# Kernel optimization log

Hardware: AMD Instinct MI355X
Metric: run time of the kernel (lower is better)

The kernel has to match this reference:

```python
import jax, jax.numpy as jnp
import numpy as np

BATCH = 16384
NUM_Q = 100000
NUM_TAGS = 1024
DIFF_FEAT = 3
DIM = 64
HIDDEN = 128


def setup_inputs() -> dict:
    key = jax.random.key(0)
    ks = jax.random.split(key, 10)
    questions = jax.random.randint(ks[0], (BATCH,), 0, NUM_Q, dtype=jnp.int64 if jax.config.jax_enable_x64 else jnp.int32)
    question_skill_targets = jax.random.randint(ks[1], (BATCH, NUM_TAGS), 0, 2, dtype=jnp.int32)
    difficulty_feats = jax.random.normal(ks[2], (BATCH, DIFF_FEAT), dtype=jnp.float32)
    Q_emb = jax.random.normal(ks[3], (NUM_Q, DIM), dtype=jnp.float32) * 0.02
    S_emb = jax.random.normal(ks[4], (NUM_TAGS, DIM), dtype=jnp.float32) * 0.02
    W_diff = jax.random.normal(ks[5], (DIFF_FEAT, DIM), dtype=jnp.float32) * 0.1
    b_diff = jnp.zeros((DIM,), dtype=jnp.float32)
    W_fc = jax.random.normal(ks[6], (3 * DIM + 3, HIDDEN), dtype=jnp.float32) * 0.05
    b_fc = jnp.zeros((HIDDEN,), dtype=jnp.float32)
    W_out = jax.random.normal(ks[7], (HIDDEN, 1), dtype=jnp.float32) * 0.05
    b_out = jnp.zeros((1,), dtype=jnp.float32)
    return {"questions": questions, "question_skill_targets": question_skill_targets,
            "difficulty_feats": difficulty_feats, "Q_emb": Q_emb, "S_emb": S_emb,
            "W_diff": W_diff, "b_diff": b_diff, "W_fc": W_fc, "b_fc": b_fc,
            "W_out": W_out, "b_out": b_out}


def reference(questions, question_skill_targets, difficulty_feats,
              Q_emb, S_emb, W_diff, b_diff, W_fc, b_fc, W_out, b_out):
    # Ragged segment-mean over skill sets: mean of skill embeddings whose
    # multi-hot entry is nonzero == (T @ S) / count per row.
    t = question_skill_targets.astype(jnp.float32)            # [B, T]
    counts = jnp.sum(t, axis=1, keepdims=True)                # [B, 1] (>=1 w.h.p.)
    mu_skill = (t @ S_emb) / counts                           # [B, D]
    q = Q_emb[questions]                                      # [B, D]
    a = difficulty_feats @ W_diff + b_diff                    # [B, D]
    # PNN product layer: pairwise inner products + concat linear signals
    p12 = jnp.sum(q * mu_skill, axis=-1, keepdims=True)
    p13 = jnp.sum(q * a, axis=-1, keepdims=True)
    p23 = jnp.sum(mu_skill * a, axis=-1, keepdims=True)
    z = jnp.concatenate([q, mu_skill, a, p12, p13, p23], axis=-1)  # [B, 3D+3]
    e = jax.nn.relu(z @ W_fc + b_fc)                          # [B, H]
    p = jax.nn.sigmoid(e @ W_out + b_out)[:, 0]               # [B]
    return (e, p)
```

## Files before the change

kernel.cpp:

```cpp
#include <hip/hip_runtime.h>
#include <hip/hip_bf16.h>

#define BATCH   16384
#define NTAGS   1024
#define DIM     64
#define HID     128

typedef __attribute__((ext_vector_type(8)))  short bf16x8;
typedef __attribute__((ext_vector_type(4)))  float f32x4;
typedef __attribute__((ext_vector_type(16))) float f32x16;

__device__ __forceinline__ unsigned short f2bf(float v) {
    unsigned u = __builtin_bit_cast(unsigned, v);
    return (unsigned short)((u + 0x7FFFu + ((u >> 16) & 1u)) >> 16);
}
__device__ __forceinline__ float bf2f(unsigned short u) {
    return __builtin_bit_cast(float, ((unsigned)u) << 16);
}

__global__ __launch_bounds__(256) void prep_pack32(const float* __restrict__ S,
                                                   const float* __restrict__ Wfc,
                                                   unsigned short* __restrict__ Sp32,
                                                   unsigned short* __restrict__ Wp)
{
    int tid = blockIdx.x * 256 + threadIdx.x;
    if (tid < 65536) {
        int k = tid >> 6, d = tid & 63;
        float v = S[tid];
        int ks = k >> 4, j = k & 7, kh = (k >> 3) & 1;
        int nf = d >> 5, lane = (d & 31) + 32 * kh;
        Sp32[((size_t)(ks * 2 + nf) * 64 + lane) * 8 + j] = f2bf(v);
    } else if (tid < 65536 + 24576) {
        int t2 = tid - 65536;
        int k = t2 >> 7, col = t2 & 127;
        float v = Wfc[t2];
        int kt = k >> 5, j = k & 7, l = ((k >> 3) & 3) * 16 + (col & 15), ct = col >> 4;
        Wp[((size_t)(kt * 8 + ct) * 64 + l) * 8 + j] = f2bf(v);
    }
}

__global__ __launch_bounds__(256) void gemm32(const int* __restrict__ T,
                                              const unsigned short* __restrict__ Sp32,
                                              unsigned short* __restrict__ musum_p,
                                              float* __restrict__ cntp)
{
    const int lane = threadIdx.x & 63;
    const int wid  = threadIdx.x >> 6;
    const int gw   = blockIdx.x * 4 + wid;
    const int mt   = gw >> 2;
    const int ksp  = gw & 3;
    const int r32  = lane & 31;
    const int kh   = lane >> 5;

    const int* tp = T + (size_t)(mt * 32 + r32) * 1024 + ksp * 256 + kh * 8;
    const unsigned short* spb = Sp32 + (size_t)(ksp * 16) * 1024 + lane * 8;

    f32x16 acc0{}, acc1{};
    int c = 0;
#pragma unroll
    for (int st = 0; st < 16; ++st) {
        int4 t0 = *(const int4*)(tp + st * 16);
        int4 t1 = *(const int4*)(tp + st * 16 + 4);
        c += t0.x + t0.y + t0.z + t0.w + t1.x + t1.y + t1.z + t1.w;
        bf16x8 af;
        af[0] = (short)((-t0.x) & 0x3F80);
        af[1] = (short)((-t0.y) & 0x3F80);
        af[2] = (short)((-t0.z) & 0x3F80);
        af[3] = (short)((-t0.w) & 0x3F80);
        af[4] = (short)((-t1.x) & 0x3F80);
        af[5] = (short)((-t1.y) & 0x3F80);
        af[6] = (short)((-t1.z) & 0x3F80);
        af[7] = (short)((-t1.w) & 0x3F80);

        const unsigned short* s2 = spb + st * 1024;
        bf16x8 b0 = *(const bf16x8*)(s2);
        bf16x8 b1 = *(const bf16x8*)(s2 + 512);

        acc0 = __builtin_amdgcn_mfma_f32_32x32x16_bf16(af, b0, acc0, 0, 0, 0);
        acc1 = __builtin_amdgcn_mfma_f32_32x32x16_bf16(af, b1, acc1, 0, 0, 0);
    }

    c += __shfl_xor(c, 32);
    if (lane < 32) cntp[(size_t)(mt * 32 + lane) * 4 + ksp] = (float)c;

    unsigned short* mo = musum_p + (size_t)ksp * BATCH * 64;
#pragma unroll
    for (int reg = 0; reg < 16; ++reg) {
        int rr = (reg & 3) + 8 * (reg >> 2) + 4 * kh;
        size_t base = (size_t)(mt * 32 + rr) * 64 + r32;
        mo[base]      = f2bf(acc0[reg]);
        mo[base + 32] = f2bf(acc1[reg]);
    }
}

__global__ __launch_bounds__(256) void tail_kernel(
    const int* __restrict__ questions, const float* __restrict__ dfeat,
    const float* __restrict__ Qemb,
    const float* __restrict__ Wdiff, const float* __restrict__ bdiff,
    const float* __restrict__ Wfc, const float* __restrict__ bfc,
    const float* __restrict__ Wout, const float* __restrict__ bout,
    const unsigned short* __restrict__ musum_p, const float* __restrict__ cntp,
    const unsigned short* __restrict__ Wp,
    float* __restrict__ out_e, float* __restrict__ out_p)
{
    __shared__ alignas(16) unsigned short zb[16][200];
    __shared__ float scal[16][3];
    __shared__ float pacc[16][4];

    const int tid  = threadIdx.x;
    const int lane = tid & 63;
    const int wid  = tid >> 6;
    const int g    = lane >> 4;
    const int rl   = lane & 15;
    const int rb   = blockIdx.x * 16;

    {
        int r = tid >> 4, c16 = tid & 15, d0 = c16 * 4;
        int row = rb + r;

        float4 cp = *(const float4*)&cntp[(size_t)row * 4];
        float inv = 1.f / (cp.x + cp.y + cp.z + cp.w);

        float m0 = 0.f, m1 = 0.f, m2 = 0.f, m3 = 0.f;
#pragma unroll
        for (int p = 0; p < 4; ++p) {
            ushort4 mv = *(const ushort4*)&musum_p[((size_t)p * BATCH + row) * 64 + d0];
            m0 += bf2f(mv.x); m1 += bf2f(mv.y); m2 += bf2f(mv.z); m3 += bf2f(mv.w);
        }
        float mu[4] = {m0 * inv, m1 * inv, m2 * inv, m3 * inv};

        int qi = questions[row];
        float4 q4 = *(const float4*)(Qemb + (size_t)qi * 64 + d0);
        float q[4] = {q4.x, q4.y, q4.z, q4.w};

        float f0 = dfeat[row * 3 + 0];
        float f1 = dfeat[row * 3 + 1];
        float f2 = dfeat[row * 3 + 2];
        float aa[4];
#pragma unroll
        for (int d = 0; d < 4; ++d)
            aa[d] = bdiff[d0 + d] + f0 * Wdiff[d0 + d] + f1 * Wdiff[64 + d0 + d]
                  + f2 * Wdiff[128 + d0 + d];

        ushort4 qv, mv, av;
        qv.x = f2bf(q[0]);  qv.y = f2bf(q[1]);  qv.z = f2bf(q[2]);  qv.w = f2bf(q[3]);
        mv.x = f2bf(mu[0]); mv.y = f2bf(mu[1]); mv.z = f2bf(mu[2]); mv.w = f2bf(mu[3]);
        av.x = f2bf(aa[0]); av.y = f2bf(aa[1]); av.z = f2bf(aa[2]); av.w = f2bf(aa[3]);
        *(ushort4*)&zb[r][d0]       = qv;
        *(ushort4*)&zb[r][64 + d0]  = mv;
        *(ushort4*)&zb[r][128 + d0] = av;

        float s12 = 0.f, s13 = 0.f, s23 = 0.f;
#pragma unroll
        for (int d = 0; d < 4; ++d) {
            s12 += q[d] * mu[d];
            s13 += q[d] * aa[d];
            s23 += mu[d] * aa[d];
        }
#pragma unroll
        for (int off = 1; off < 16; off <<= 1) {
            s12 += __shfl_xor(s12, off);
            s13 += __shfl_xor(s13, off);
            s23 += __shfl_xor(s23, off);
        }
        if (c16 == 0) { scal[r][0] = s12; scal[r][1] = s13; scal[r][2] = s23; }
    }
    __syncthreads();

    {
        bf16x8 afr[6];
#pragma unroll
        for (int kt = 0; kt < 6; ++kt)
            afr[kt] = *(const bf16x8*)&zb[rl][kt * 32 + g * 8];

        float pr0 = 0.f, pr1 = 0.f, pr2 = 0.f, pr3 = 0.f;
#pragma unroll
        for (int c2 = 0; c2 < 2; ++c2) {
            int ct = wid * 2 + c2;
            f32x4 e{};
            const unsigned short* wp = Wp + (size_t)ct * 512 + lane * 8;
#pragma unroll
            for (int kt = 0; kt < 6; ++kt) {
                bf16x8 bfr = *(const bf16x8*)(wp + (size_t)kt * 4096);
                e = __builtin_amdgcn_mfma_f32_16x16x32_bf16(afr[kt], bfr, e, 0, 0, 0);
            }
            int h = ct * 16 + rl;
            float w192 = Wfc[192 * 128 + h];
            float w193 = Wfc[193 * 128 + h];
            float w194 = Wfc[194 * 128 + h];
            float bb = bfc[h];
            float wo = Wout[h];
#pragma unroll
            for (int r = 0; r < 4; ++r) {
                int row = g * 4 + r;
                float ev = e[r] + bb + scal[row][0] * w192 + scal[row][1] * w193
                         + scal[row][2] * w194;
                ev = ev > 0.f ? ev : 0.f;
                out_e[(size_t)(rb + row) * 128 + h] = ev;
                float pc = ev * wo;
                if (r == 0) pr0 += pc; else if (r == 1) pr1 += pc;
                else if (r == 2) pr2 += pc; else pr3 += pc;
            }
        }
#pragma unroll
        for (int off = 1; off < 16; off <<= 1) {
            pr0 += __shfl_xor(pr0, off);
            pr1 += __shfl_xor(pr1, off);
            pr2 += __shfl_xor(pr2, off);
            pr3 += __shfl_xor(pr3, off);
        }
        if (rl == 0) {
            pacc[g * 4 + 0][wid] = pr0;
            pacc[g * 4 + 1][wid] = pr1;
            pacc[g * 4 + 2][wid] = pr2;
            pacc[g * 4 + 3][wid] = pr3;
        }
    }
    __syncthreads();
    if (tid < 16) {
        float v = pacc[tid][0] + pacc[tid][1] + pacc[tid][2] + pacc[tid][3] + bout[0];
        out_p[rb + tid] = 1.f / (1.f + expf(-v));
    }
}

extern "C" void kernel_launch(void* const* d_in, const int* in_sizes, int n_in,
                              void* d_out, int out_size, void* d_ws, size_t ws_size,
                              hipStream_t stream)
{
    const int*   questions = (const int*)d_in[0];
    const int*   T         = (const int*)d_in[1];
    const float* dfeat     = (const float*)d_in[2];
    const float* Qemb      = (const float*)d_in[3];
    const float* Semb      = (const float*)d_in[4];
    const float* Wdiff     = (const float*)d_in[5];
    const float* bdiff     = (const float*)d_in[6];
    const float* Wfc       = (const float*)d_in[7];
    const float* bfc       = (const float*)d_in[8];
    const float* Wout      = (const float*)d_in[9];
    const float* bout      = (const float*)d_in[10];

    char* ws = (char*)d_ws;
    unsigned short* Sp32    = (unsigned short*)ws;
    unsigned short* Wp      = (unsigned short*)(ws + 131072);
    unsigned short* musum_p = (unsigned short*)(ws + 262144);
    float*          cntp    = (float*)(ws + 262144 + 8388608);

    float* out_e = (float*)d_out;
    float* out_p = out_e + (size_t)BATCH * HID;

    hipLaunchKernelGGL(prep_pack32, dim3(352), dim3(256), 0, stream, Semb, Wfc, Sp32, Wp);
    hipLaunchKernelGGL(gemm32, dim3(512), dim3(256), 0, stream, T, Sp32, musum_p, cntp);
    hipLaunchKernelGGL(tail_kernel, dim3(BATCH / 16), dim3(256), 0, stream,
                       questions, dfeat, Qemb, Wdiff, bdiff, Wfc, bfc, Wout, bout,
                       musum_p, cntp, Wp, out_e, out_p);
}
```

Measured before the change: 31.67 us.

## Fuse skill GEMM and MLP tail into one kernel with LDS partial sums

Merges the multi-hot-times-skill-embedding GEMM and the MLP tail into a single 512-thread kernel handling 32 rows per block. Eight waves each cover a 128-wide K slice and reduce their partial sums through LDS, so the bf16 partial-sum buffer no longer goes to global memory and one launch is removed. Question-embedding and difficulty-feature loads are issued before the GEMM to overlap their latency. In exchange there are fewer blocks (512), larger LDS use per block, and a barrier between the GEMM and tail phases.

```diff
diff --git a/kernel.cpp b/kernel.cpp
--- a/kernel.cpp
+++ b/kernel.cpp
@@ -39,108 +39,98 @@
     }
 }
 
-__global__ __launch_bounds__(256) void gemm32(const int* __restrict__ T,
-                                              const unsigned short* __restrict__ Sp32,
-                                              unsigned short* __restrict__ musum_p,
-                                              float* __restrict__ cntp)
-{
-    const int lane = threadIdx.x & 63;
-    const int wid  = threadIdx.x >> 6;
-    const int gw   = blockIdx.x * 4 + wid;
-    const int mt   = gw >> 2;
-    const int ksp  = gw & 3;
-    const int r32  = lane & 31;
-    const int kh   = lane >> 5;
-
-    const int* tp = T + (size_t)(mt * 32 + r32) * 1024 + ksp * 256 + kh * 8;
-    const unsigned short* spb = Sp32 + (size_t)(ksp * 16) * 1024 + lane * 8;
-
-    f32x16 acc0{}, acc1{};
-    int c = 0;
-#pragma unroll
-    for (int st = 0; st < 16; ++st) {
-        int4 t0 = *(const int4*)(tp + st * 16);
-        int4 t1 = *(const int4*)(tp + st * 16 + 4);
-        c += t0.x + t0.y + t0.z + t0.w + t1.x + t1.y + t1.z + t1.w;
-        bf16x8 af;
-        af[0] = (short)((-t0.x) & 0x3F80);
-        af[1] = (short)((-t0.y) & 0x3F80);
-        af[2] = (short)((-t0.z) & 0x3F80);
-        af[3] = (short)((-t0.w) & 0x3F80);
-        af[4] = (short)((-t1.x) & 0x3F80);
-        af[5] = (short)((-t1.y) & 0x3F80);
-        af[6] = (short)((-t1.z) & 0x3F80);
-        af[7] = (short)((-t1.w) & 0x3F80);
-
-        const unsigned short* s2 = spb + st * 1024;
-        bf16x8 b0 = *(const bf16x8*)(s2);
-        bf16x8 b1 = *(const bf16x8*)(s2 + 512);
-
-        acc0 = __builtin_amdgcn_mfma_f32_32x32x16_bf16(af, b0, acc0, 0, 0, 0);
-        acc1 = __builtin_amdgcn_mfma_f32_32x32x16_bf16(af, b1, acc1, 0, 0, 0);
-    }
-
-    c += __shfl_xor(c, 32);
-    if (lane < 32) cntp[(size_t)(mt * 32 + lane) * 4 + ksp] = (float)c;
-
-    unsigned short* mo = musum_p + (size_t)ksp * BATCH * 64;
-#pragma unroll
-    for (int reg = 0; reg < 16; ++reg) {
-        int rr = (reg & 3) + 8 * (reg >> 2) + 4 * kh;
-        size_t base = (size_t)(mt * 32 + rr) * 64 + r32;
-        mo[base]      = f2bf(acc0[reg]);
-        mo[base + 32] = f2bf(acc1[reg]);
-    }
-}
-
-__global__ __launch_bounds__(256) void tail_kernel(
-    const int* __restrict__ questions, const float* __restrict__ dfeat,
-    const float* __restrict__ Qemb,
+__global__ __launch_bounds__(512, 4) void fused_kernel(
+    const int* __restrict__ questions, const int* __restrict__ T,
+    const float* __restrict__ dfeat, const float* __restrict__ Qemb,
     const float* __restrict__ Wdiff, const float* __restrict__ bdiff,
     const float* __restrict__ Wfc, const float* __restrict__ bfc,
     const float* __restrict__ Wout, const float* __restrict__ bout,
-    const unsigned short* __restrict__ musum_p, const float* __restrict__ cntp,
-    const unsigned short* __restrict__ Wp,
+    const unsigned short* __restrict__ Sp32, const unsigned short* __restrict__ Wp,
     float* __restrict__ out_e, float* __restrict__ out_p)
 {
-    __shared__ alignas(16) unsigned short zb[16][200];
-    __shared__ float scal[16][3];
-    __shared__ float pacc[16][4];
+    __shared__ alignas(16) unsigned short accp[8][32][72];
+    __shared__ float cntp[8][32];
+    __shared__ alignas(16) unsigned short zb[32][200];
+    __shared__ float scal[32][3];
+    __shared__ float pacc[32][4];
 
     const int tid  = threadIdx.x;
     const int lane = tid & 63;
     const int wid  = tid >> 6;
+    const int r32  = lane & 31;
+    const int kh   = lane >> 5;
     const int g    = lane >> 4;
     const int rl   = lane & 15;
-    const int rb   = blockIdx.x * 16;
+    const int rb   = blockIdx.x * 32;
+
+    const int pr_r = tid >> 4, pr_c = tid & 15, pr_d0 = pr_c * 4;
+    const int qi = questions[rb + pr_r];
+    const float4 q4 = *(const float4*)(Qemb + (size_t)qi * 64 + pr_d0);
+    const float pf0 = dfeat[(rb + pr_r) * 3 + 0];
+    const float pf1 = dfeat[(rb + pr_r) * 3 + 1];
+    const float pf2 = dfeat[(rb + pr_r) * 3 + 2];
 
     {
-        int r = tid >> 4, c16 = tid & 15, d0 = c16 * 4;
-        int row = rb + r;
-
-        float4 cp = *(const float4*)&cntp[(size_t)row * 4];
-        float inv = 1.f / (cp.x + cp.y + cp.z + cp.w);
+        f32x16 acc0{}, acc1{};
+        int c = 0;
+        const int* tp = T + (size_t)(rb + r32) * 1024 + wid * 128 + kh * 8;
+        const unsigned short* spb = Sp32 + (size_t)(wid * 8) * 1024 + lane * 8;
+
+#pragma unroll
+        for (int st = 0; st < 8; ++st) {
+            int4 t0 = *(const int4*)(tp + st * 16);
+            int4 t1 = *(const int4*)(tp + st * 16 + 4);
+            c += t0.x + t0.y + t0.z + t0.w + t1.x + t1.y + t1.z + t1.w;
+            bf16x8 af;
+            af[0] = (short)((-t0.x) & 0x3F80);
+            af[1] = (short)((-t0.y) & 0x3F80);
+            af[2] = (short)((-t0.z) & 0x3F80);
+            af[3] = (short)((-t0.w) & 0x3F80);
+            af[4] = (short)((-t1.x) & 0x3F80);
+            af[5] = (short)((-t1.y) & 0x3F80);
+            af[6] = (short)((-t1.z) & 0x3F80);
+            af[7] = (short)((-t1.w) & 0x3F80);
+
+            const unsigned short* s2 = spb + st * 1024;
+            bf16x8 b0 = *(const bf16x8*)(s2);
+            bf16x8 b1 = *(const bf16x8*)(s2 + 512);
+
+            acc0 = __builtin_amdgcn_mfma_f32_32x32x16_bf16(af, b0, acc0, 0, 0, 0);
+            acc1 = __builtin_amdgcn_mfma_f32_32x32x16_bf16(af, b1, acc1, 0, 0, 0);
+        }
+
+        c += __shfl_xor(c, 32);
+        if (lane < 32) cntp[wid][lane] = (float)c;
+
+#pragma unroll
+        for (int reg = 0; reg < 16; ++reg) {
+            int rr = (reg & 3) + 8 * (reg >> 2) + 4 * kh;
+            accp[wid][rr][r32]      = f2bf(acc0[reg]);
+            accp[wid][rr][32 + r32] = f2bf(acc1[reg]);
+        }
+    }
+    __syncthreads();
+
+    {
+        int r = pr_r, c16 = pr_c, d0 = pr_d0;
+        float cc = 0.f;
+#pragma unroll
+        for (int p = 0; p < 8; ++p) cc += cntp[p][r];
+        float inv = 1.f / cc;
 
         float m0 = 0.f, m1 = 0.f, m2 = 0.f, m3 = 0.f;
 #pragma unroll
-        for (int p = 0; p < 4; ++p) {
-            ushort4 mv = *(const ushort4*)&musum_p[((size_t)p * BATCH + row) * 64 + d0];
+        for (int p = 0; p < 8; ++p) {
+            ushort4 mv = *(const ushort4*)&accp[p][r][d0];
             m0 += bf2f(mv.x); m1 += bf2f(mv.y); m2 += bf2f(mv.z); m3 += bf2f(mv.w);
         }
         float mu[4] = {m0 * inv, m1 * inv, m2 * inv, m3 * inv};
-
-        int qi = questions[row];
-        float4 q4 = *(const float4*)(Qemb + (size_t)qi * 64 + d0);
         float q[4] = {q4.x, q4.y, q4.z, q4.w};
-
-        float f0 = dfeat[row * 3 + 0];
-        float f1 = dfeat[row * 3 + 1];
-        float f2 = dfeat[row * 3 + 2];
         float aa[4];
 #pragma unroll
         for (int d = 0; d < 4; ++d)
-            aa[d] = bdiff[d0 + d] + f0 * Wdiff[d0 + d] + f1 * Wdiff[64 + d0 + d]
-                  + f2 * Wdiff[128 + d0 + d];
+            aa[d] = bdiff[d0 + d] + pf0 * Wdiff[d0 + d] + pf1 * Wdiff[64 + d0 + d]
+                  + pf2 * Wdiff[128 + d0 + d];
 
         ushort4 qv, mv, av;
         qv.x = f2bf(q[0]);  qv.y = f2bf(q[1]);  qv.z = f2bf(q[2]);  qv.w = f2bf(q[3]);
@@ -168,15 +158,18 @@
     __syncthreads();
 
     {
+        const int rh    = wid >> 2;
+        const int cpair = wid & 3;
+
         bf16x8 afr[6];
 #pragma unroll
         for (int kt = 0; kt < 6; ++kt)
-            afr[kt] = *(const bf16x8*)&zb[rl][kt * 32 + g * 8];
+            afr[kt] = *(const bf16x8*)&zb[rh * 16 + rl][kt * 32 + g * 8];
 
         float pr0 = 0.f, pr1 = 0.f, pr2 = 0.f, pr3 = 0.f;
 #pragma unroll
         for (int c2 = 0; c2 < 2; ++c2) {
-            int ct = wid * 2 + c2;
+            int ct = cpair * 2 + c2;
             f32x4 e{};
             const unsigned short* wp = Wp + (size_t)ct * 512 + lane * 8;
 #pragma unroll
@@ -192,11 +185,11 @@
             float wo = Wout[h];
 #pragma unroll
             for (int r = 0; r < 4; ++r) {
-                int row = g * 4 + r;
-                float ev = e[r] + bb + scal[row][0] * w192 + scal[row][1] * w193
-                         + scal[row][2] * w194;
+                int lr = rh * 16 + g * 4 + r;
+                float ev = e[r] + bb + scal[lr][0] * w192 + scal[lr][1] * w193
+                         + scal[lr][2] * w194;
                 ev = ev > 0.f ? ev : 0.f;
-                out_e[(size_t)(rb + row) * 128 + h] = ev;
+                out_e[(size_t)(rb + lr) * 128 + h] = ev;
                 float pc = ev * wo;
                 if (r == 0) pr0 += pc; else if (r == 1) pr1 += pc;
                 else if (r == 2) pr2 += pc; else pr3 += pc;
@@ -210,14 +203,14 @@
             pr3 += __shfl_xor(pr3, off);
         }
         if (rl == 0) {
-            pacc[g * 4 + 0][wid] = pr0;
-            pacc[g * 4 + 1][wid] = pr1;
-            pacc[g * 4 + 2][wid] = pr2;
-            pacc[g * 4 + 3][wid] = pr3;
+            pacc[rh * 16 + g * 4 + 0][cpair] = pr0;
+            pacc[rh * 16 + g * 4 + 1][cpair] = pr1;
+            pacc[rh * 16 + g * 4 + 2][cpair] = pr2;
+            pacc[rh * 16 + g * 4 + 3][cpair] = pr3;
         }
     }
     __syncthreads();
-    if (tid < 16) {
+    if (tid < 32) {
         float v = pacc[tid][0] + pacc[tid][1] + pacc[tid][2] + pacc[tid][3] + bout[0];
         out_p[rb + tid] = 1.f / (1.f + expf(-v));
     }
@@ -240,17 +233,14 @@
     const float* bout      = (const float*)d_in[10];
 
     char* ws = (char*)d_ws;
-    unsigned short* Sp32    = (unsigned short*)ws;
-    unsigned short* Wp      = (unsigned short*)(ws + 131072);
-    unsigned short* musum_p = (unsigned short*)(ws + 262144);
-    float*          cntp    = (float*)(ws + 262144 + 8388608);
+    unsigned short* Sp32 = (unsigned short*)ws;
+    unsigned short* Wp   = (unsigned short*)(ws + 131072);
 
     float* out_e = (float*)d_out;
     float* out_p = out_e + (size_t)BATCH * HID;
 
     hipLaunchKernelGGL(prep_pack32, dim3(352), dim3(256), 0, stream, Semb, Wfc, Sp32, Wp);
-    hipLaunchKernelGGL(gemm32, dim3(512), dim3(256), 0, stream, T, Sp32, musum_p, cntp);
-    hipLaunchKernelGGL(tail_kernel, dim3(BATCH / 16), dim3(256), 0, stream,
-                       questions, dfeat, Qemb, Wdiff, bdiff, Wfc, bfc, Wout, bout,
-                       musum_p, cntp, Wp, out_e, out_p);
-}
+    hipLaunchKernelGGL(fused_kernel, dim3(BATCH / 32), dim3(512), 0, stream,
+                       questions, T, dfeat, Qemb, Wdiff, bdiff, Wfc, bfc, Wout, bout,
+                       Sp32, Wp, out_e, out_p);
+}
```

Result: faster. 29.31 us (-7.4%).
